# Kernel tuning notes

Hardware: AMD Instinct MI355X
Metric: run time of the kernel (lower is better)

## Reference

```python
import jax, jax.numpy as jnp
import numpy as np

B, S, E, H, L, V = 4, 2048, 512, 8, 2, 32000
D = E // H
FF = 4 * E


def make_pos_emb(max_len, embed_dim):
    pos = np.arange(max_len, dtype=np.float32)[:, None]
    den = np.exp(np.arange(0, embed_dim, 2, dtype=np.float32) / embed_dim * np.log(10000.0))
    pe = np.zeros((max_len, embed_dim), dtype=np.float32)
    pe[:, 0::2] = np.sin(pos / den)
    pe[:, 1::2] = np.cos(pos / den)
    return jnp.asarray(pe)


def setup_inputs() -> dict:
    key = jax.random.key(0)
    ks = jax.random.split(key, 12)
    scale = 0.02
    inp = {
        'x': jax.random.randint(ks[0], (B, S), 0, V, dtype=jnp.int32),
        'mask': jax.random.randint(ks[1], (B, 1, 1, S), 0, 2, dtype=jnp.int32),
        'emb': jax.random.normal(ks[2], (V, E), dtype=jnp.float32) * scale,
        'pos_emb': make_pos_emb(S, E),
        'Wq': jax.random.normal(ks[3], (L, E, E), dtype=jnp.float32) * scale,
        'Wk': jax.random.normal(ks[4], (L, E, E), dtype=jnp.float32) * scale,
        'Wv': jax.random.normal(ks[5], (L, E, E), dtype=jnp.float32) * scale,
        'Wo': jax.random.normal(ks[6], (L, E, E), dtype=jnp.float32) * scale,
        'bo': jnp.zeros((L, E), jnp.float32),
        'ln1_g': jnp.ones((L, E), jnp.float32),
        'ln1_b': jnp.zeros((L, E), jnp.float32),
        'ln2_g': jnp.ones((L, E), jnp.float32),
        'ln2_b': jnp.zeros((L, E), jnp.float32),
        'Wf1': jax.random.normal(ks[7], (L, FF, E), dtype=jnp.float32) * scale,
        'bf1': jnp.zeros((L, FF), jnp.float32),
        'Wf2': jax.random.normal(ks[8], (L, E, FF), dtype=jnp.float32) * scale,
        'bf2': jnp.zeros((L, E), jnp.float32),
    }
    return inp


def _layer_norm(x, g, b, eps=1e-5):
    m = jnp.mean(x, axis=-1, keepdims=True)
    v = jnp.mean(jnp.square(x - m), axis=-1, keepdims=True)
    return (x - m) * jax.lax.rsqrt(v + eps) * g + b


def _encoder(x, mask, emb, pos_emb, Wq, Wk, Wv, Wo, bo, ln1_g, ln1_b, ln2_g, ln2_b, Wf1, bf1, Wf2, bf2):
    # embedding + sinusoidal positional encoding (dropout is identity in eval)
    h = emb[x] + pos_emb[None, :S]  # (B, S, E)
    # NOTE: original scales scores by sqrt(d_k) where d_k is the KEY LENGTH
    inv_scale = 1.0 / jnp.sqrt(jnp.float32(S))
    neg = jnp.float32(-1e20)
    for l in range(L):
        q = (h @ Wq[l].T).reshape(B, S, H, D)
        k = (h @ Wk[l].T).reshape(B, S, H, D)
        v = (h @ Wv[l].T).reshape(B, S, H, D)
        energy = jnp.einsum('nqhd,nkhd->nhqk', q, k)  # (B, H, S, S)
        energy = jnp.where(mask == 0, neg, energy)
        attn = jax.nn.softmax(energy * inv_scale, axis=-1)
        o = jnp.einsum('nhql,nlhd->nqhd', attn, v).reshape(B, S, E)
        o = o @ Wo[l].T + bo[l]
        h1 = _layer_norm(o + h, ln1_g[l], ln1_b[l])
        ff = jax.nn.relu(h1 @ Wf1[l].T + bf1[l]) @ Wf2[l].T + bf2[l]
        h = _layer_norm(ff + h1, ln2_g[l], ln2_b[l])
    return h


def reference(x, mask, emb, pos_emb, Wq, Wk, Wv, Wo, bo, ln1_g, ln1_b, ln2_g, ln2_b, Wf1, bf1, Wf2, bf2):
    return _encoder(x, mask, emb, pos_emb, Wq, Wk, Wv, Wo, bo, ln1_g, ln1_b, ln2_g, ln2_b, Wf1, bf1, Wf2, bf2)
```

## Files before the change

### kernel.cpp

```cpp
#include <hip/hip_runtime.h>
#include <math.h>

#define BATCH 4
#define SEQ   2048
#define EDIM  512
#define NH    8
#define HD    64
#define FFD   2048
#define NLAYER 2
#define MTOK  (BATCH * SEQ)
#define MEL   ((long long)MTOK * EDIM)

typedef __attribute__((ext_vector_type(8))) short bf16x8;
typedef __attribute__((ext_vector_type(4))) float f32x4;

__device__ __forceinline__ unsigned short f2bf(float f) {
  unsigned u = __float_as_uint(f);
  u += 0x7fffu + ((u >> 16) & 1u);
  return (unsigned short)(u >> 16);
}
__device__ __forceinline__ float bf2f(unsigned short h) {
  return __uint_as_float(((unsigned)h) << 16);
}
__device__ __forceinline__ void splitf(float v, unsigned short* hi, unsigned short* lo) {
  unsigned short h = f2bf(v);
  *hi = h;
  *lo = f2bf(v - bf2f(h));
}

__global__ __launch_bounds__(256) void embed_kernel(
    const int* __restrict__ x, const float* __restrict__ emb,
    const float* __restrict__ pos, float* __restrict__ h,
    unsigned short* __restrict__ h2)
{
  int idx = blockIdx.x * 256 + threadIdx.x;
  int t = idx >> 7;
  int c = idx & 127;
  int s = t & (SEQ - 1);
  int v = x[t];
  float4 ev = ((const float4*)emb)[(long long)v * 128 + c];
  float4 pv = ((const float4*)pos)[(long long)s * 128 + c];
  float4 r;
  r.x = ev.x + pv.x; r.y = ev.y + pv.y; r.z = ev.z + pv.z; r.w = ev.w + pv.w;
  ((float4*)h)[idx] = r;

  ushort4 hi, lo;
  splitf(r.x, &hi.x, &lo.x); splitf(r.y, &hi.y, &lo.y);
  splitf(r.z, &hi.z, &lo.z); splitf(r.w, &hi.w, &lo.w);
  size_t base = ((size_t)t << 10) + (size_t)c * 4;
  *(ushort4*)&h2[base] = hi;
  *(ushort4*)&h2[base + EDIM] = lo;
}

__global__ __launch_bounds__(256) void split_kernel(
    const float* __restrict__ src, unsigned short* __restrict__ dst, int shift)
{
  int idx = blockIdx.x * 256 + threadIdx.x;
  int row = idx >> shift;
  int c4 = idx & ((1 << shift) - 1);
  int Koff = 4 << shift;
  float4 v = ((const float4*)src)[idx];
  ushort4 hi, lo;
  splitf(v.x, &hi.x, &lo.x); splitf(v.y, &hi.y, &lo.y);
  splitf(v.z, &hi.z, &lo.z); splitf(v.w, &hi.w, &lo.w);
  size_t base = ((size_t)row << (shift + 3)) + (size_t)c4 * 4;
  *(ushort4*)&dst[base] = hi;
  *(ushort4*)&dst[base + Koff] = lo;
}

__global__ __launch_bounds__(256) void gemm_split(
    const unsigned short* __restrict__ A,
    const unsigned short* __restrict__ B0,
    const unsigned short* __restrict__ B1,
    const unsigned short* __restrict__ B2,
    void* __restrict__ Cbase, long long czstride,
    const float* __restrict__ bias,
    int N, int K, int outmode, int relu, int chunks)
{
  __shared__ unsigned short As[128 * 64];
  __shared__ unsigned short Bs[128 * 64];

  const int tid = threadIdx.x;
  const int lane = tid & 63;
  const int wid = tid >> 6;
  const int wr = wid >> 1, wc = wid & 1;
  const int fl = lane & 15;
  const int kg = lane >> 4;
  const int z = blockIdx.z;
  const unsigned short* __restrict__ B = (z == 0) ? B0 : ((z == 1) ? B1 : B2);
  const int brow = blockIdx.y * 128;
  const int bcol = blockIdx.x * 128;
  const int ld = 2 * K;

  f32x4 acc[4][4];
#pragma unroll
  for (int i = 0; i < 4; ++i)
#pragma unroll
    for (int j = 0; j < 4; ++j) acc[i][j] = (f32x4){0.f, 0.f, 0.f, 0.f};

  const int r0 = lane >> 3;
  const int c0 = (lane & 7) * 8;

  for (int kt = 0; kt < chunks * K; kt += 64) {
    const int akt = (kt < 2 * K) ? kt : kt - 2 * K;
    const int bkt = (kt < K) ? kt : kt - K;
#pragma unroll
    for (int i = 0; i < 4; ++i) {
      const int chunk = i * 4 + wid;
      const int r = chunk * 8 + r0;
      const unsigned short* ga = A + (size_t)(brow + r) * ld + akt + c0;
      const unsigned short* gb = B + (size_t)(bcol + r) * ld + bkt + c0;
      __builtin_amdgcn_global_load_lds(
          (const __attribute__((address_space(1))) void*)ga,
          (__attribute__((address_space(3))) void*)&As[chunk * 512 + lane * 8],
          16, 0, 0);
      __builtin_amdgcn_global_load_lds(
          (const __attribute__((address_space(1))) void*)gb,
          (__attribute__((address_space(3))) void*)&Bs[chunk * 512 + lane * 8],
          16, 0, 0);
    }
    __syncthreads();
#pragma unroll
    for (int kk = 0; kk < 2; ++kk) {
      bf16x8 av[4], bv[4];
#pragma unroll
      for (int f = 0; f < 4; ++f) {
        av[f] = *(const bf16x8*)&As[(wr * 64 + f * 16 + fl) * 64 + kk * 32 + kg * 8];
        bv[f] = *(const bf16x8*)&Bs[(wc * 64 + f * 16 + fl) * 64 + kk * 32 + kg * 8];
      }
#pragma unroll
      for (int i = 0; i < 4; ++i)
#pragma unroll
        for (int j = 0; j < 4; ++j)
          acc[i][j] = __builtin_amdgcn_mfma_f32_16x16x32_bf16(av[i], bv[j], acc[i][j], 0, 0, 0);
    }
    __syncthreads();
  }

  if (outmode == 0) {
    float* C = (float*)Cbase + (size_t)z * czstride;
#pragma unroll
    for (int j = 0; j < 4; ++j) {
      const int col = bcol + wc * 64 + j * 16 + fl;
      const float bb = bias ? bias[col] : 0.f;
#pragma unroll
      for (int i = 0; i < 4; ++i) {
        const int rowb = brow + wr * 64 + i * 16 + kg * 4;
#pragma unroll
        for (int e = 0; e < 4; ++e) {
          float v = acc[i][j][e] + bb;
          if (relu) v = fmaxf(v, 0.f);
          C[(size_t)(rowb + e) * N + col] = v;
        }
      }
    }
  } else if (outmode == 1) {
    unsigned short* C = (unsigned short*)Cbase + (size_t)z * czstride;
#pragma unroll
    for (int j = 0; j < 4; ++j) {
      const int col = bcol + wc * 64 + j * 16 + fl;
      const float bb = bias ? bias[col] : 0.f;
#pragma unroll
      for (int i = 0; i < 4; ++i) {
        const int rowb = brow + wr * 64 + i * 16 + kg * 4;
#pragma unroll
        for (int e = 0; e < 4; ++e) {
          float v = acc[i][j][e] + bb;
          if (relu) v = fmaxf(v, 0.f);
          unsigned short hi, lo;
          splitf(v, &hi, &lo);
          size_t rb = (size_t)(rowb + e) * (2 * (size_t)N);
          C[rb + col] = hi;
          C[rb + N + col] = lo;
        }
      }
    }
  } else {
    unsigned short* C = (unsigned short*)Cbase + (size_t)z * czstride;
#pragma unroll
    for (int j = 0; j < 4; ++j) {
      const int col = bcol + wc * 64 + j * 16 + fl;
      const float bb = bias ? bias[col] : 0.f;
#pragma unroll
      for (int i = 0; i < 4; ++i) {
        const int rowb = brow + wr * 64 + i * 16 + kg * 4;
#pragma unroll
        for (int e = 0; e < 4; ++e) {
          float v = acc[i][j][e] + bb;
          if (relu) v = fmaxf(v, 0.f);
          C[(size_t)(rowb + e) * N + col] = f2bf(v);
        }
      }
    }
  }
}

__global__ __launch_bounds__(256, 2) void attn_mfma(
    const unsigned short* __restrict__ q2,
    const unsigned short* __restrict__ k2,
    const unsigned short* __restrict__ v2t,
    const int* __restrict__ maskg,
    unsigned short* __restrict__ o2)
{
  __shared__ unsigned short Ps[128 * 40];

  const int tid = threadIdx.x;
  const int lane = tid & 63;
  const int wid = tid >> 6;
  const int fl = lane & 15;
  const int kg = lane >> 4;
  const int b = blockIdx.y >> 3, h = blockIdx.y & 7;
  const int hc = h * 64;
  const int q0w = blockIdx.x * 128 + wid * 32;
  const float inv_scale = 0.022097086912079608f;
  const size_t bS = (size_t)b * SEQ;

  bf16x8 aq[2][2];
#pragma unroll
  for (int rg = 0; rg < 2; ++rg) {
    size_t qr = (bS + q0w + rg * 16 + fl) * 512 + hc + kg * 8;
    aq[rg][0] = *(const bf16x8*)&q2[qr];
    aq[rg][1] = *(const bf16x8*)&q2[qr + 32];
  }

  const unsigned short* kp0 = k2 + (bS + fl) * 512 + hc + kg * 8;
  const unsigned short* kp1 = k2 + (bS + 16 + fl) * 512 + hc + kg * 8;
  const unsigned short* vbp[4];
#pragma unroll
  for (int cf = 0; cf < 4; ++cf)
    vbp[cf] = v2t + (size_t)(hc + cf * 16 + fl) * 8192 + bS + kg * 8;
  const int* mrow = maskg + bS;

  float m[2][4], l[2][4];
  f32x4 ov[2][4];
#pragma unroll
  for (int rg = 0; rg < 2; ++rg) {
#pragma unroll
    for (int e = 0; e < 4; ++e) { m[rg][e] = -INFINITY; l[rg][e] = 0.f; }
#pragma unroll
    for (int cf = 0; cf < 4; ++cf) ov[rg][cf] = (f32x4){0.f, 0.f, 0.f, 0.f};
  }

  auto ldk = [&](bf16x8 (&kf)[4], int k0) {
    size_t kr = (size_t)k0 * 512;
    kf[0] = *(const bf16x8*)(kp0 + kr);
    kf[1] = *(const bf16x8*)(kp0 + kr + 32);
    kf[2] = *(const bf16x8*)(kp1 + kr);
    kf[3] = *(const bf16x8*)(kp1 + kr + 32);
  };
  auto ldv = [&](bf16x8 (&vf)[4], int k0) {
#pragma unroll
    for (int cf = 0; cf < 4; ++cf)
      vf[cf] = *(const bf16x8*)(vbp[cf] + k0);
  };

  auto tile = [&](const bf16x8 (&kf)[4], const bf16x8 (&vf)[4], int k0) {
    const bool dead0 = (mrow[k0 + fl] == 0);
    const bool dead1 = (mrow[k0 + 16 + fl] == 0);

    f32x4 sc[2][2];
#pragma unroll
    for (int rg = 0; rg < 2; ++rg)
#pragma unroll
      for (int cf = 0; cf < 2; ++cf) sc[rg][cf] = (f32x4){0.f, 0.f, 0.f, 0.f};

#pragma unroll
    for (int c = 0; c < 2; ++c) {
      sc[0][0] = __builtin_amdgcn_mfma_f32_16x16x32_bf16(aq[0][c], kf[c], sc[0][0], 0, 0, 0);
      sc[1][0] = __builtin_amdgcn_mfma_f32_16x16x32_bf16(aq[1][c], kf[c], sc[1][0], 0, 0, 0);
      sc[0][1] = __builtin_amdgcn_mfma_f32_16x16x32_bf16(aq[0][c], kf[2 + c], sc[0][1], 0, 0, 0);
      sc[1][1] = __builtin_amdgcn_mfma_f32_16x16x32_bf16(aq[1][c], kf[2 + c], sc[1][1], 0, 0, 0);
    }

#pragma unroll
    for (int rg = 0; rg < 2; ++rg) {
#pragma unroll
      for (int e = 0; e < 4; ++e) {
        float s0 = dead0 ? -1e20f : sc[rg][0][e];
        float s1 = dead1 ? -1e20f : sc[rg][1][e];
        sc[rg][0][e] = s0 * inv_scale;
        sc[rg][1][e] = s1 * inv_scale;
      }
#pragma unroll
      for (int e = 0; e < 4; ++e) {
        float rm = fmaxf(sc[rg][0][e], sc[rg][1][e]);
        rm = fmaxf(rm, __shfl_xor(rm, 1));
        rm = fmaxf(rm, __shfl_xor(rm, 2));
        rm = fmaxf(rm, __shfl_xor(rm, 4));
        rm = fmaxf(rm, __shfl_xor(rm, 8));
        float mnew = fmaxf(m[rg][e], rm);
        float corr = __expf(m[rg][e] - mnew);
        float p0 = __expf(sc[rg][0][e] - mnew);
        float p1 = __expf(sc[rg][1][e] - mnew);
        sc[rg][0][e] = p0; sc[rg][1][e] = p1;
        float ps = p0 + p1;
        ps += __shfl_xor(ps, 1); ps += __shfl_xor(ps, 2);
        ps += __shfl_xor(ps, 4); ps += __shfl_xor(ps, 8);
        l[rg][e] = l[rg][e] * corr + ps;
        m[rg][e] = mnew;
#pragma unroll
        for (int cf = 0; cf < 4; ++cf) ov[rg][cf][e] *= corr;
      }
#pragma unroll
      for (int cf = 0; cf < 2; ++cf)
#pragma unroll
        for (int e = 0; e < 4; ++e) {
          int prow = wid * 32 + rg * 16 + kg * 4 + e;
          Ps[prow * 40 + cf * 16 + fl] = f2bf(sc[rg][cf][e]);
        }
    }

    bf16x8 ap0 = *(const bf16x8*)&Ps[(wid * 32 + fl) * 40 + kg * 8];
    bf16x8 ap1 = *(const bf16x8*)&Ps[(wid * 32 + 16 + fl) * 40 + kg * 8];
#pragma unroll
    for (int cf = 0; cf < 4; ++cf) {
      ov[0][cf] = __builtin_amdgcn_mfma_f32_16x16x32_bf16(ap0, vf[cf], ov[0][cf], 0, 0, 0);
      ov[1][cf] = __builtin_amdgcn_mfma_f32_16x16x32_bf16(ap1, vf[cf], ov[1][cf], 0, 0, 0);
    }
  };

  bf16x8 ka[4], kb[4], va[4], vc[4];
  ldk(ka, 0);
  for (int k0 = 0; k0 < SEQ; k0 += 64) {
    ldv(va, k0);
    ldk(kb, k0 + 32);
    tile(ka, va, k0);
    ldv(vc, k0 + 32);
    ldk(ka, k0 + 64);
    tile(kb, vc, k0 + 32);
  }

#pragma unroll
  for (int rg = 0; rg < 2; ++rg)
#pragma unroll
    for (int e = 0; e < 4; ++e) {
      float inv = 1.0f / l[rg][e];
      size_t trow = (bS + q0w + rg * 16 + kg * 4 + e) * 1024 + hc;
#pragma unroll
      for (int cf = 0; cf < 4; ++cf) {
        float v = ov[rg][cf][e] * inv;
        unsigned short hi = f2bf(v);
        unsigned short lo = f2bf(v - bf2f(hi));
        o2[trow + cf * 16 + fl] = hi;
        o2[trow + 512 + cf * 16 + fl] = lo;
      }
    }
}

__global__ __launch_bounds__(128) void ln_res_kernel(
    const float* __restrict__ X, const float* __restrict__ R,
    const float* __restrict__ g, const float* __restrict__ be,
    float* __restrict__ out, unsigned short* __restrict__ out2)
{
  const int row = blockIdx.x;
  const int tid = threadIdx.x;
  const long long off = (long long)row * EDIM + tid * 4;
  float4 xv = *(const float4*)&X[off];
  float4 rv = *(const float4*)&R[off];
  float x0 = xv.x + rv.x, x1 = xv.y + rv.y, x2 = xv.z + rv.z, x3 = xv.w + rv.w;

  __shared__ float red[2];
  float s = (x0 + x1) + (x2 + x3);
#pragma unroll
  for (int o2 = 1; o2 < 64; o2 <<= 1) s += __shfl_xor(s, o2);
  if ((tid & 63) == 0) red[tid >> 6] = s;
  __syncthreads();
  float mean = (red[0] + red[1]) * (1.0f / EDIM);

  float d0 = x0 - mean, d1 = x1 - mean, d2 = x2 - mean, d3 = x3 - mean;
  float s2 = (d0 * d0 + d1 * d1) + (d2 * d2 + d3 * d3);
#pragma unroll
  for (int o2 = 1; o2 < 64; o2 <<= 1) s2 += __shfl_xor(s2, o2);
  __syncthreads();
  if ((tid & 63) == 0) red[tid >> 6] = s2;
  __syncthreads();
  float var = (red[0] + red[1]) * (1.0f / EDIM);
  float rstd = rsqrtf(var + 1e-5f);

  float4 gv = *(const float4*)&g[tid * 4];
  float4 bv = *(const float4*)&be[tid * 4];
  float4 ov;
  ov.x = d0 * rstd * gv.x + bv.x;
  ov.y = d1 * rstd * gv.y + bv.y;
  ov.z = d2 * rstd * gv.z + bv.z;
  ov.w = d3 * rstd * gv.w + bv.w;
  *(float4*)&out[off] = ov;

  if (out2) {
    ushort4 hi, lo;
    splitf(ov.x, &hi.x, &lo.x); splitf(ov.y, &hi.y, &lo.y);
    splitf(ov.z, &hi.z, &lo.z); splitf(ov.w, &hi.w, &lo.w);
    size_t b2 = ((size_t)row << 10) + (size_t)tid * 4;
    *(ushort4*)&out2[b2] = hi;
    *(ushort4*)&out2[b2 + EDIM] = lo;
  }
}

extern "C" void kernel_launch(void* const* d_in, const int* in_sizes, int n_in,
                              void* d_out, int out_size, void* d_ws, size_t ws_size,
                              hipStream_t stream) {
  (void)in_sizes; (void)n_in; (void)out_size; (void)ws_size;

  const int*   x    = (const int*)d_in[0];
  const int*   mask = (const int*)d_in[1];
  const float* emb  = (const float*)d_in[2];
  const float* pos  = (const float*)d_in[3];
  const float* Wq   = (const float*)d_in[4];
  const float* Wk   = (const float*)d_in[5];
  const float* Wv   = (const float*)d_in[6];
  const float* Wo   = (const float*)d_in[7];
  const float* bo   = (const float*)d_in[8];
  const float* ln1g = (const float*)d_in[9];
  const float* ln1b = (const float*)d_in[10];
  const float* ln2g = (const float*)d_in[11];
  const float* ln2b = (const float*)d_in[12];
  const float* Wf1  = (const float*)d_in[13];
  const float* bf1  = (const float*)d_in[14];
  const float* Wf2  = (const float*)d_in[15];
  const float* bf2  = (const float*)d_in[16];
  float* out = (float*)d_out;

  float* hb = (float*)d_ws;
  float* h1 = hb + MEL;
  unsigned short* q2  = (unsigned short*)(hb + 2 * MEL);
  unsigned short* k2  = q2 + (size_t)MTOK * 512;
  unsigned short* v2t = k2 + (size_t)MTOK * 512;
  float* t1 = (float*)(hb + 2 * MEL);
  unsigned short* ff2 = (unsigned short*)(hb + 2 * MEL);
  unsigned short* act2 = (unsigned short*)(hb + 6 * MEL);
  unsigned short* wq2  = act2 + (size_t)MTOK * 1024;
  unsigned short* wk2  = wq2 + 512 * 1024;
  unsigned short* wv2  = wk2 + 512 * 1024;
  unsigned short* wo2  = wv2 + 512 * 1024;
  unsigned short* wf12 = wo2 + 512 * 1024;
  unsigned short* wf22 = wf12 + (size_t)2048 * 1024;

  embed_kernel<<<dim3(MTOK * (EDIM / 4) / 256), 256, 0, stream>>>(x, emb, pos, hb, act2);

  for (int l = 0; l < NLAYER; ++l) {
    const float* wq = Wq + (long long)l * EDIM * EDIM;
    const float* wk = Wk + (long long)l * EDIM * EDIM;
    const float* wv = Wv + (long long)l * EDIM * EDIM;
    const float* wo = Wo + (long long)l * EDIM * EDIM;
    const float* wf1 = Wf1 + (long long)l * FFD * EDIM;
    const float* wf2 = Wf2 + (long long)l * EDIM * FFD;

    split_kernel<<<dim3(256), 256, 0, stream>>>(wq, wq2, 7);
    split_kernel<<<dim3(256), 256, 0, stream>>>(wk, wk2, 7);
    split_kernel<<<dim3(256), 256, 0, stream>>>(wv, wv2, 7);
    split_kernel<<<dim3(256), 256, 0, stream>>>(wo, wo2, 7);
    split_kernel<<<dim3(1024), 256, 0, stream>>>(wf1, wf12, 7);
    split_kernel<<<dim3(1024), 256, 0, stream>>>(wf2, wf22, 9);

    gemm_split<<<dim3(EDIM / 128, MTOK / 128, 2), 256, 0, stream>>>(
        act2, wq2, wk2, nullptr, q2, (long long)MTOK * 512, nullptr,
        EDIM, EDIM, 2, 0, 1);

    gemm_split<<<dim3(MTOK / 128, EDIM / 128, 1), 256, 0, stream>>>(
        wv2, act2, nullptr, nullptr, v2t, 0, nullptr,
        MTOK, EDIM, 2, 0, 1);

    attn_mfma<<<dim3(SEQ / 128, BATCH * NH), 256, 0, stream>>>(
        q2, k2, v2t, mask, act2);

    gemm_split<<<dim3(EDIM / 128, MTOK / 128, 1), 256, 0, stream>>>(
        act2, wo2, nullptr, nullptr, t1, 0, bo + (long long)l * EDIM,
        EDIM, EDIM, 0, 0, 3);

    ln_res_kernel<<<MTOK, 128, 0, stream>>>(
        t1, hb, ln1g + (long long)l * EDIM, ln1b + (long long)l * EDIM, h1, act2);

    gemm_split<<<dim3(FFD / 128, MTOK / 128, 1), 256, 0, stream>>>(
        act2, wf12, nullptr, nullptr, ff2, 0, bf1 + (long long)l * FFD,
        FFD, EDIM, 1, 1, 3);

    gemm_split<<<dim3(EDIM / 128, MTOK / 128, 1), 256, 0, stream>>>(
        ff2, wf22, nullptr, nullptr, hb, 0, bf2 + (long long)l * EDIM,
        EDIM, FFD, 0, 0, 3);

    float* lnout = (l == NLAYER - 1) ? out : hb;
    unsigned short* lnout2 = (l == NLAYER - 1) ? nullptr : act2;
    ln_res_kernel<<<MTOK, 128, 0, stream>>>(
        hb, h1, ln2g + (long long)l * EDIM, ln2b + (long long)l * EDIM, lnout, lnout2);
  }
}
```

Before: 1.046 ms.

## Run FFN GEMMs in single-pass fp16 and shrink attention query tile

Replaces the split-bf16 (hi/lo, three-chunk) FFN GEMMs with a plain fp16 MFMA GEMM. Weights are converted to fp16 and LayerNorm-1 emits an fp16 copy of its output, so each FFN GEMM does one MFMA pass instead of three and moves half the operand bytes. The attention kernel now handles 64 queries per block (16 per wave) with higher launch-bound occupancy, giving more blocks and fewer registers per wave. The cost is lower precision in the FFN path, and the attention kernel reloads K/V more often relative to the queries it processes.

```diff
diff --git a/kernel.cpp b/kernel.cpp
--- a/kernel.cpp
+++ b/kernel.cpp
@@ -13,6 +13,8 @@
 
 typedef __attribute__((ext_vector_type(8))) short bf16x8;
 typedef __attribute__((ext_vector_type(4))) float f32x4;
+typedef __attribute__((ext_vector_type(8))) _Float16 f16x8;
+typedef __attribute__((ext_vector_type(4))) _Float16 f16x4;
 
 __device__ __forceinline__ unsigned short f2bf(float f) {
   unsigned u = __float_as_uint(f);
@@ -66,6 +68,15 @@
   size_t base = ((size_t)row << (shift + 3)) + (size_t)c4 * 4;
   *(ushort4*)&dst[base] = hi;
   *(ushort4*)&dst[base + Koff] = lo;
+}
+
+__global__ __launch_bounds__(256) void tofp16_kernel(
+    const float* __restrict__ src, _Float16* __restrict__ dst)
+{
+  int idx = blockIdx.x * 256 + threadIdx.x;
+  float4 v = ((const float4*)src)[idx];
+  *(f16x4*)&dst[(size_t)idx * 4] =
+      (f16x4){(_Float16)v.x, (_Float16)v.y, (_Float16)v.z, (_Float16)v.w};
 }
 
 __global__ __launch_bounds__(256) void gemm_split(
@@ -195,14 +206,113 @@
   }
 }
 
-__global__ __launch_bounds__(256, 2) void attn_mfma(
+__global__ __launch_bounds__(256) void gemm_f16(
+    const _Float16* __restrict__ A,
+    const _Float16* __restrict__ B,
+    void* __restrict__ Cbase,
+    const float* __restrict__ bias,
+    int N, int K, int outmode, int relu)
+{
+  __shared__ _Float16 As[128 * 64];
+  __shared__ _Float16 Bs[128 * 64];
+
+  const int tid = threadIdx.x;
+  const int lane = tid & 63;
+  const int wid = tid >> 6;
+  const int wr = wid >> 1, wc = wid & 1;
+  const int fl = lane & 15;
+  const int kg = lane >> 4;
+  const int brow = blockIdx.y * 128;
+  const int bcol = blockIdx.x * 128;
+
+  f32x4 acc[4][4];
+#pragma unroll
+  for (int i = 0; i < 4; ++i)
+#pragma unroll
+    for (int j = 0; j < 4; ++j) acc[i][j] = (f32x4){0.f, 0.f, 0.f, 0.f};
+
+  const int r0 = lane >> 3;
+  const int c0 = (lane & 7) * 8;
+
+  for (int kt = 0; kt < K; kt += 64) {
+#pragma unroll
+    for (int i = 0; i < 4; ++i) {
+      const int chunk = i * 4 + wid;
+      const int r = chunk * 8 + r0;
+      const _Float16* ga = A + (size_t)(brow + r) * K + kt + c0;
+      const _Float16* gb = B + (size_t)(bcol + r) * K + kt + c0;
+      __builtin_amdgcn_global_load_lds(
+          (const __attribute__((address_space(1))) void*)ga,
+          (__attribute__((address_space(3))) void*)&As[chunk * 512 + lane * 8],
+          16, 0, 0);
+      __builtin_amdgcn_global_load_lds(
+          (const __attribute__((address_space(1))) void*)gb,
+          (__attribute__((address_space(3))) void*)&Bs[chunk * 512 + lane * 8],
+          16, 0, 0);
+    }
+    __syncthreads();
+#pragma unroll
+    for (int kk = 0; kk < 2; ++kk) {
+      f16x8 av[4], bv[4];
+#pragma unroll
+      for (int f = 0; f < 4; ++f) {
+        av[f] = *(const f16x8*)&As[(wr * 64 + f * 16 + fl) * 64 + kk * 32 + kg * 8];
+        bv[f] = *(const f16x8*)&Bs[(wc * 64 + f * 16 + fl) * 64 + kk * 32 + kg * 8];
+      }
+#pragma unroll
+      for (int i = 0; i < 4; ++i)
+#pragma unroll
+        for (int j = 0; j < 4; ++j)
+          acc[i][j] = __builtin_amdgcn_mfma_f32_16x16x32_f16(av[i], bv[j], acc[i][j], 0, 0, 0);
+    }
+    __syncthreads();
+  }
+
+  if (outmode == 0) {
+    float* C = (float*)Cbase;
+#pragma unroll
+    for (int j = 0; j < 4; ++j) {
+      const int col = bcol + wc * 64 + j * 16 + fl;
+      const float bb = bias ? bias[col] : 0.f;
+#pragma unroll
+      for (int i = 0; i < 4; ++i) {
+        const int rowb = brow + wr * 64 + i * 16 + kg * 4;
+#pragma unroll
+        for (int e = 0; e < 4; ++e) {
+          float v = acc[i][j][e] + bb;
+          if (relu) v = fmaxf(v, 0.f);
+          C[(size_t)(rowb + e) * N + col] = v;
+        }
+      }
+    }
+  } else {
+    _Float16* C = (_Float16*)Cbase;
+#pragma unroll
+    for (int j = 0; j < 4; ++j) {
+      const int col = bcol + wc * 64 + j * 16 + fl;
+      const float bb = bias ? bias[col] : 0.f;
+#pragma unroll
+      for (int i = 0; i < 4; ++i) {
+        const int rowb = brow + wr * 64 + i * 16 + kg * 4;
+#pragma unroll
+        for (int e = 0; e < 4; ++e) {
+          float v = acc[i][j][e] + bb;
+          if (relu) v = fmaxf(v, 0.f);
+          C[(size_t)(rowb + e) * N + col] = (_Float16)v;
+        }
+      }
+    }
+  }
+}
+
+__global__ __launch_bounds__(256, 4) void attn_mfma(
     const unsigned short* __restrict__ q2,
     const unsigned short* __restrict__ k2,
     const unsigned short* __restrict__ v2t,
     const int* __restrict__ maskg,
     unsigned short* __restrict__ o2)
 {
-  __shared__ unsigned short Ps[128 * 40];
+  __shared__ unsigned short Ps[64 * 40];
 
   const int tid = threadIdx.x;
   const int lane = tid & 63;
@@ -211,16 +321,15 @@
   const int kg = lane >> 4;
   const int b = blockIdx.y >> 3, h = blockIdx.y & 7;
   const int hc = h * 64;
-  const int q0w = blockIdx.x * 128 + wid * 32;
+  const int q0w = blockIdx.x * 64 + wid * 16;
   const float inv_scale = 0.022097086912079608f;
   const size_t bS = (size_t)b * SEQ;
 
-  bf16x8 aq[2][2];
-#pragma unroll
-  for (int rg = 0; rg < 2; ++rg) {
-    size_t qr = (bS + q0w + rg * 16 + fl) * 512 + hc + kg * 8;
-    aq[rg][0] = *(const bf16x8*)&q2[qr];
-    aq[rg][1] = *(const bf16x8*)&q2[qr + 32];
+  bf16x8 aq[2];
+  {
+    size_t qr = (bS + q0w + fl) * 512 + hc + kg * 8;
+    aq[0] = *(const bf16x8*)&q2[qr];
+    aq[1] = *(const bf16x8*)&q2[qr + 32];
   }
 
   const unsigned short* kp0 = k2 + (bS + fl) * 512 + hc + kg * 8;
@@ -231,15 +340,12 @@
     vbp[cf] = v2t + (size_t)(hc + cf * 16 + fl) * 8192 + bS + kg * 8;
   const int* mrow = maskg + bS;
 
-  float m[2][4], l[2][4];
-  f32x4 ov[2][4];
-#pragma unroll
-  for (int rg = 0; rg < 2; ++rg) {
-#pragma unroll
-    for (int e = 0; e < 4; ++e) { m[rg][e] = -INFINITY; l[rg][e] = 0.f; }
-#pragma unroll
-    for (int cf = 0; cf < 4; ++cf) ov[rg][cf] = (f32x4){0.f, 0.f, 0.f, 0.f};
-  }
+  float m[4], l[4];
+  f32x4 ov[4];
+#pragma unroll
+  for (int e = 0; e < 4; ++e) { m[e] = -INFINITY; l[e] = 0.f; }
+#pragma unroll
+  for (int cf = 0; cf < 4; ++cf) ov[cf] = (f32x4){0.f, 0.f, 0.f, 0.f};
 
   auto ldk = [&](bf16x8 (&kf)[4], int k0) {
     size_t kr = (size_t)k0 * 512;
@@ -258,65 +364,54 @@
     const bool dead0 = (mrow[k0 + fl] == 0);
     const bool dead1 = (mrow[k0 + 16 + fl] == 0);
 
-    f32x4 sc[2][2];
-#pragma unroll
-    for (int rg = 0; rg < 2; ++rg)
-#pragma unroll
-      for (int cf = 0; cf < 2; ++cf) sc[rg][cf] = (f32x4){0.f, 0.f, 0.f, 0.f};
-
+    f32x4 sc[2];
+    sc[0] = (f32x4){0.f, 0.f, 0.f, 0.f};
+    sc[1] = (f32x4){0.f, 0.f, 0.f, 0.f};
 #pragma unroll
     for (int c = 0; c < 2; ++c) {
-      sc[0][0] = __builtin_amdgcn_mfma_f32_16x16x32_bf16(aq[0][c], kf[c], sc[0][0], 0, 0, 0);
-      sc[1][0] = __builtin_amdgcn_mfma_f32_16x16x32_bf16(aq[1][c], kf[c], sc[1][0], 0, 0, 0);
-      sc[0][1] = __builtin_amdgcn_mfma_f32_16x16x32_bf16(aq[0][c], kf[2 + c], sc[0][1], 0, 0, 0);
-      sc[1][1] = __builtin_amdgcn_mfma_f32_16x16x32_bf16(aq[1][c], kf[2 + c], sc[1][1], 0, 0, 0);
-    }
-
-#pragma unroll
-    for (int rg = 0; rg < 2; ++rg) {
+      sc[0] = __builtin_amdgcn_mfma_f32_16x16x32_bf16(aq[c], kf[c], sc[0], 0, 0, 0);
+      sc[1] = __builtin_amdgcn_mfma_f32_16x16x32_bf16(aq[c], kf[2 + c], sc[1], 0, 0, 0);
+    }
+
+#pragma unroll
+    for (int e = 0; e < 4; ++e) {
+      float s0 = dead0 ? -1e20f : sc[0][e];
+      float s1 = dead1 ? -1e20f : sc[1][e];
+      sc[0][e] = s0 * inv_scale;
+      sc[1][e] = s1 * inv_scale;
+    }
+#pragma unroll
+    for (int e = 0; e < 4; ++e) {
+      float rm = fmaxf(sc[0][e], sc[1][e]);
+      rm = fmaxf(rm, __shfl_xor(rm, 1));
+      rm = fmaxf(rm, __shfl_xor(rm, 2));
+      rm = fmaxf(rm, __shfl_xor(rm, 4));
+      rm = fmaxf(rm, __shfl_xor(rm, 8));
+      float mnew = fmaxf(m[e], rm);
+      float corr = __expf(m[e] - mnew);
+      float p0 = __expf(sc[0][e] - mnew);
+      float p1 = __expf(sc[1][e] - mnew);
+      sc[0][e] = p0; sc[1][e] = p1;
+      float ps = p0 + p1;
+      ps += __shfl_xor(ps, 1); ps += __shfl_xor(ps, 2);
+      ps += __shfl_xor(ps, 4); ps += __shfl_xor(ps, 8);
+      l[e] = l[e] * corr + ps;
+      m[e] = mnew;
+#pragma unroll
+      for (int cf = 0; cf < 4; ++cf) ov[cf][e] *= corr;
+    }
+#pragma unroll
+    for (int cf = 0; cf < 2; ++cf)
 #pragma unroll
       for (int e = 0; e < 4; ++e) {
-        float s0 = dead0 ? -1e20f : sc[rg][0][e];
-        float s1 = dead1 ? -1e20f : sc[rg][1][e];
-        sc[rg][0][e] = s0 * inv_scale;
-        sc[rg][1][e] = s1 * inv_scale;
-      }
-#pragma unroll
-      for (int e = 0; e < 4; ++e) {
-        float rm = fmaxf(sc[rg][0][e], sc[rg][1][e]);
-        rm = fmaxf(rm, __shfl_xor(rm, 1));
-        rm = fmaxf(rm, __shfl_xor(rm, 2));
-        rm = fmaxf(rm, __shfl_xor(rm, 4));
-        rm = fmaxf(rm, __shfl_xor(rm, 8));
-        float mnew = fmaxf(m[rg][e], rm);
-        float corr = __expf(m[rg][e] - mnew);
-        float p0 = __expf(sc[rg][0][e] - mnew);
-        float p1 = __expf(sc[rg][1][e] - mnew);
-        sc[rg][0][e] = p0; sc[rg][1][e] = p1;
-        float ps = p0 + p1;
-        ps += __shfl_xor(ps, 1); ps += __shfl_xor(ps, 2);
-        ps += __shfl_xor(ps, 4); ps += __shfl_xor(ps, 8);
-        l[rg][e] = l[rg][e] * corr + ps;
-        m[rg][e] = mnew;
-#pragma unroll
-        for (int cf = 0; cf < 4; ++cf) ov[rg][cf][e] *= corr;
-      }
-#pragma unroll
-      for (int cf = 0; cf < 2; ++cf)
-#pragma unroll
-        for (int e = 0; e < 4; ++e) {
-          int prow = wid * 32 + rg * 16 + kg * 4 + e;
-          Ps[prow * 40 + cf * 16 + fl] = f2bf(sc[rg][cf][e]);
-        }
-    }
-
-    bf16x8 ap0 = *(const bf16x8*)&Ps[(wid * 32 + fl) * 40 + kg * 8];
-    bf16x8 ap1 = *(const bf16x8*)&Ps[(wid * 32 + 16 + fl) * 40 + kg * 8];
-#pragma unroll
-    for (int cf = 0; cf < 4; ++cf) {
-      ov[0][cf] = __builtin_amdgcn_mfma_f32_16x16x32_bf16(ap0, vf[cf], ov[0][cf], 0, 0, 0);
-      ov[1][cf] = __builtin_amdgcn_mfma_f32_16x16x32_bf16(ap1, vf[cf], ov[1][cf], 0, 0, 0);
-    }
+        int prow = wid * 16 + kg * 4 + e;
+        Ps[prow * 40 + cf * 16 + fl] = f2bf(sc[cf][e]);
+      }
+
+    bf16x8 ap = *(const bf16x8*)&Ps[(wid * 16 + fl) * 40 + kg * 8];
+#pragma unroll
+    for (int cf = 0; cf < 4; ++cf)
+      ov[cf] = __builtin_amdgcn_mfma_f32_16x16x32_bf16(ap, vf[cf], ov[cf], 0, 0, 0);
   };
 
   bf16x8 ka[4], kb[4], va[4], vc[4];
@@ -331,26 +426,25 @@
   }
 
 #pragma unroll
-  for (int rg = 0; rg < 2; ++rg)
-#pragma unroll
-    for (int e = 0; e < 4; ++e) {
-      float inv = 1.0f / l[rg][e];
-      size_t trow = (bS + q0w + rg * 16 + kg * 4 + e) * 1024 + hc;
-#pragma unroll
-      for (int cf = 0; cf < 4; ++cf) {
-        float v = ov[rg][cf][e] * inv;
-        unsigned short hi = f2bf(v);
-        unsigned short lo = f2bf(v - bf2f(hi));
-        o2[trow + cf * 16 + fl] = hi;
-        o2[trow + 512 + cf * 16 + fl] = lo;
-      }
-    }
+  for (int e = 0; e < 4; ++e) {
+    float inv = 1.0f / l[e];
+    size_t trow = (bS + q0w + kg * 4 + e) * 1024 + hc;
+#pragma unroll
+    for (int cf = 0; cf < 4; ++cf) {
+      float v = ov[cf][e] * inv;
+      unsigned short hi = f2bf(v);
+      unsigned short lo = f2bf(v - bf2f(hi));
+      o2[trow + cf * 16 + fl] = hi;
+      o2[trow + 512 + cf * 16 + fl] = lo;
+    }
+  }
 }
 
 __global__ __launch_bounds__(128) void ln_res_kernel(
     const float* __restrict__ X, const float* __restrict__ R,
     const float* __restrict__ g, const float* __restrict__ be,
-    float* __restrict__ out, unsigned short* __restrict__ out2)
+    float* __restrict__ out, unsigned short* __restrict__ out2,
+    _Float16* __restrict__ outh)
 {
   const int row = blockIdx.x;
   const int tid = threadIdx.x;
@@ -393,6 +487,10 @@
     size_t b2 = ((size_t)row << 10) + (size_t)tid * 4;
     *(ushort4*)&out2[b2] = hi;
     *(ushort4*)&out2[b2 + EDIM] = lo;
+  }
+  if (outh) {
+    *(f16x4*)&outh[(size_t)row * EDIM + tid * 4] =
+        (f16x4){(_Float16)ov.x, (_Float16)ov.y, (_Float16)ov.z, (_Float16)ov.w};
   }
 }
 
@@ -426,7 +524,8 @@
   unsigned short* k2  = q2 + (size_t)MTOK * 512;
   unsigned short* v2t = k2 + (size_t)MTOK * 512;
   float* t1 = (float*)(hb + 2 * MEL);
-  unsigned short* ff2 = (unsigned short*)(hb + 2 * MEL);
+  _Float16* h1f  = (_Float16*)(hb + 3 * MEL + MEL / 2);
+  _Float16* ff1h = (_Float16*)(hb + 4 * MEL);
   unsigned short* act2 = (unsigned short*)(hb + 6 * MEL);
   unsigned short* wq2  = act2 + (size_t)MTOK * 1024;
   unsigned short* wk2  = wq2 + 512 * 1024;
@@ -434,6 +533,8 @@
   unsigned short* wo2  = wv2 + 512 * 1024;
   unsigned short* wf12 = wo2 + 512 * 1024;
   unsigned short* wf22 = wf12 + (size_t)2048 * 1024;
+  _Float16* wf1h = (_Float16*)wf12;
+  _Float16* wf2h = (_Float16*)wf22;
 
   embed_kernel<<<dim3(MTOK * (EDIM / 4) / 256), 256, 0, stream>>>(x, emb, pos, hb, act2);
 
@@ -449,8 +550,8 @@
     split_kernel<<<dim3(256), 256, 0, stream>>>(wk, wk2, 7);
     split_kernel<<<dim3(256), 256, 0, stream>>>(wv, wv2, 7);
     split_kernel<<<dim3(256), 256, 0, stream>>>(wo, wo2, 7);
-    split_kernel<<<dim3(1024), 256, 0, stream>>>(wf1, wf12, 7);
-    split_kernel<<<dim3(1024), 256, 0, stream>>>(wf2, wf22, 9);
+    tofp16_kernel<<<dim3(1024), 256, 0, stream>>>(wf1, wf1h);
+    tofp16_kernel<<<dim3(1024), 256, 0, stream>>>(wf2, wf2h);
 
     gemm_split<<<dim3(EDIM / 128, MTOK / 128, 2), 256, 0, stream>>>(
         act2, wq2, wk2, nullptr, q2, (long long)MTOK * 512, nullptr,
@@ -460,7 +561,7 @@
         wv2, act2, nullptr, nullptr, v2t, 0, nullptr,
         MTOK, EDIM, 2, 0, 1);
 
-    attn_mfma<<<dim3(SEQ / 128, BATCH * NH), 256, 0, stream>>>(
+    attn_mfma<<<dim3(SEQ / 64, BATCH * NH), 256, 0, stream>>>(
         q2, k2, v2t, mask, act2);
 
     gemm_split<<<dim3(EDIM / 128, MTOK / 128, 1), 256, 0, stream>>>(
@@ -468,19 +569,19 @@
         EDIM, EDIM, 0, 0, 3);
 
     ln_res_kernel<<<MTOK, 128, 0, stream>>>(
-        t1, hb, ln1g + (long long)l * EDIM, ln1b + (long long)l * EDIM, h1, act2);
-
-    gemm_split<<<dim3(FFD / 128, MTOK / 128, 1), 256, 0, stream>>>(
-        act2, wf12, nullptr, nullptr, ff2, 0, bf1 + (long long)l * FFD,
-        FFD, EDIM, 1, 1, 3);
-
-    gemm_split<<<dim3(EDIM / 128, MTOK / 128, 1), 256, 0, stream>>>(
-        ff2, wf22, nullptr, nullptr, hb, 0, bf2 + (long long)l * EDIM,
-        EDIM, FFD, 0, 0, 3);
+        t1, hb, ln1g + (long long)l * EDIM, ln1b + (long long)l * EDIM,
+        h1, nullptr, h1f);
+
+    gemm_f16<<<dim3(FFD / 128, MTOK / 128), 256, 0, stream>>>(
+        h1f, wf1h, ff1h, bf1 + (long long)l * FFD, FFD, EDIM, 1, 1);
+
+    gemm_f16<<<dim3(EDIM / 128, MTOK / 128), 256, 0, stream>>>(
+        ff1h, wf2h, hb, bf2 + (long long)l * EDIM, EDIM, FFD, 0, 0);
 
     float* lnout = (l == NLAYER - 1) ? out : hb;
     unsigned short* lnout2 = (l == NLAYER - 1) ? nullptr : act2;
     ln_res_kernel<<<MTOK, 128, 0, stream>>>(
-        hb, h1, ln2g + (long long)l * EDIM, ln2b + (long long)l * EDIM, lnout, lnout2);
-  }
-}
+        hb, h1, ln2g + (long long)l * EDIM, ln2b + (long long)l * EDIM,
+        lnout, lnout2, nullptr);
+  }
+}
```

New measurement: 987.3 us. 1.06x faster.
